# Kernel tuning notes

Hardware: AMD Instinct MI355X
Metric: run time of the kernel (lower is better)

## Reference

```python
import jax, jax.numpy as jnp
import numpy as np
import math

N_HEAD = 8


def _rope(x):
    # x: [B, H, S, D]; lucidrains rotary_embedding_torch default: interleaved pairs, theta=10000
    D = x.shape[-1]
    S = x.shape[-2]
    inv_freq = 1.0 / (10000.0 ** (jnp.arange(0, D, 2, dtype=jnp.float32) / D))  # [D/2]
    t = jnp.arange(S, dtype=jnp.float32)
    freqs = jnp.repeat(t[:, None] * inv_freq[None, :], 2, axis=-1)  # [S, D] interleaved repeat
    cos = jnp.cos(freqs).astype(x.dtype)
    sin = jnp.sin(freqs).astype(x.dtype)
    xp = x.reshape(*x.shape[:-1], D // 2, 2)
    rot = jnp.stack((-xp[..., 1], xp[..., 0]), axis=-1).reshape(x.shape)  # rotate_half (interleaved)
    return x * cos + rot * sin


def _row_linear(x, Wo):
    # faithful RowLinear: transpose then flat-reshape back (a real permutation), linear, inverse shuffle
    B, S, P = x.shape
    E = Wo.shape[0]
    x = jnp.swapaxes(x, 1, 2).reshape(B, S, P)
    x = jnp.einsum('bsp,ep->bse', x, Wo)  # [B, S, E]
    x = x.reshape(B, E, -1)  # [B, E, S]
    return jnp.swapaxes(x, 1, 2)  # [B, S, E]


def setup_inputs() -> dict:
    key = jax.random.key(0)
    k0, k1, k2, k3, k4 = jax.random.split(key, 5)
    B, S, E, P = 4, 2048, 1024, 1024
    std = 1.0 / math.sqrt(E)
    return {
        'emb': jax.random.normal(k0, (B, S, E), dtype=jnp.float32),
        'W1': jax.random.normal(k1, (P, E), dtype=jnp.float32) * std,
        'W2': jax.random.normal(k2, (P, E), dtype=jnp.float32) * std,
        'W3': jax.random.normal(k3, (P, E), dtype=jnp.float32) * std,
        'Wo': jax.random.normal(k4, (E, P), dtype=jnp.float32) * std,
    }


def reference(emb, W1, W2, W3, Wo):
    B, S, E = emb.shape
    P = W1.shape[0]
    H = N_HEAD
    D = P // H
    q = jnp.einsum('bse,pe->bsp', emb, W1).reshape(B, H, S, D)  # raw view split (as in source)
    k = jnp.einsum('bse,pe->bsp', emb, W2).reshape(B, H, S, D)
    v = jnp.einsum('bse,pe->bsp', emb, W3).reshape(B, H, S, D)
    q = _rope(q)
    k = _rope(k)
    scores = jnp.einsum('bhqd,bhkd->bhqk', q, k).astype(jnp.float32) / math.sqrt(H)
    attn = jax.nn.softmax(scores, axis=-1).astype(v.dtype)
    out = jnp.einsum('bhqk,bhkd->bhqd', attn, v)  # [B, H, S, D]
    out = jnp.swapaxes(out, 1, 2).reshape(B, S, P)
    return _row_linear(out, Wo)
```

## Files before the change

### kernel.cpp

```cpp
#include <hip/hip_runtime.h>

typedef float f32x4 __attribute__((ext_vector_type(4)));
typedef __bf16 bf16x8 __attribute__((ext_vector_type(8)));

__device__ __forceinline__ unsigned short f2bf(float f) {
  unsigned int u = __float_as_uint(f);
  u = (u + 0x7FFFu + ((u >> 16) & 1u)) >> 16;
  return (unsigned short)u;
}

__device__ __forceinline__ f32x4 mfma16(bf16x8 a, bf16x8 b, f32x4 c) {
  return __builtin_amdgcn_mfma_f32_16x16x32_bf16(a, b, c, 0, 0, 0);
}

__device__ __forceinline__ void load8_bf16(const unsigned short* p, unsigned short* d) {
  *(uint4*)d = *(const uint4*)p;
}
__device__ __forceinline__ void load8_bf16(const float* p, unsigned short* d) {
  float4 a = *(const float4*)p;
  float4 b = *(const float4*)(p + 4);
  __align__(16) unsigned short t[8] = {f2bf(a.x), f2bf(a.y), f2bf(a.z), f2bf(a.w),
                                       f2bf(b.x), f2bf(b.y), f2bf(b.z), f2bf(b.w)};
  *(uint4*)d = *(uint4*)t;
}

__device__ __forceinline__ void gload_lds16(const unsigned short* g, unsigned short* l) {
  __builtin_amdgcn_global_load_lds(
      (const __attribute__((address_space(1))) void*)g,
      (__attribute__((address_space(3))) void*)l, 16, 0, 0);
}

__global__ __launch_bounds__(256) void convert_gen(const float* __restrict__ src,
                                                   unsigned short* __restrict__ dst) {
  int idx = (blockIdx.x * 256 + threadIdx.x) * 8;
  __align__(16) unsigned short t[8];
  load8_bf16(src + idx, t);
  *(uint4*)(dst + idx) = *(uint4*)t;
}

__global__ __launch_bounds__(256) void convert_w3(const float* __restrict__ W1,
                                                  const float* __restrict__ W2,
                                                  const float* __restrict__ W3,
                                                  unsigned short* __restrict__ dst) {
  int i = blockIdx.x;
  int sel = i >> 9;
  const float* src = (sel == 0) ? W1 : (sel == 1) ? W2 : W3;
  int off = (i & 511) * 2048 + threadIdx.x * 8;
  __align__(16) unsigned short t[8];
  load8_bf16(src + off, t);
  *(uint4*)(dst + sel * 1048576 + off) = *(uint4*)t;
}

__global__ __launch_bounds__(256) void gemm_qkv(const unsigned short* __restrict__ A,
                                                const unsigned short* __restrict__ WB,
                                                unsigned short* __restrict__ q,
                                                unsigned short* __restrict__ k,
                                                unsigned short* __restrict__ v) {
  __shared__ __align__(16) unsigned short As[128][32];
  __shared__ __align__(16) unsigned short Bs[128][32];
  const int t = threadIdx.x;
  const int lane = t & 63;
  const int wid = t >> 6;
  const int quad = lane >> 4;
  const int l16 = lane & 15;
  const int wm = (wid >> 1) << 6;
  const int wn = (wid & 1) << 6;
  const int sel = blockIdx.x >> 3;
  const int nb = (blockIdx.x & 7) << 7;
  const int mbase = blockIdx.y * 128;
  const unsigned short* Bt = WB + sel * 1048576;
  unsigned short* C = (sel == 0) ? q : (sel == 1) ? k : v;

  f32x4 acc[4][4] = {};

  for (int k0 = 0; k0 < 1024; k0 += 32) {
#pragma unroll
    for (int i = 0; i < 2; ++i) {
      int c = t + (i << 8);
      int row = c >> 2;
      int col = (c & 3) << 3;
      gload_lds16(A + (size_t)(mbase + row) * 1024 + k0 + col, &As[row][col]);
      gload_lds16(Bt + (size_t)(nb + row) * 1024 + k0 + col, &Bs[row][col]);
    }
    __syncthreads();
    bf16x8 af[4], bfr[4];
#pragma unroll
    for (int mt = 0; mt < 4; ++mt)
      af[mt] = *(const bf16x8*)(&As[wm + mt * 16 + l16][quad * 8]);
#pragma unroll
    for (int nt = 0; nt < 4; ++nt)
      bfr[nt] = *(const bf16x8*)(&Bs[wn + nt * 16 + l16][quad * 8]);
#pragma unroll
    for (int mt = 0; mt < 4; ++mt)
#pragma unroll
      for (int nt = 0; nt < 4; ++nt)
        acc[mt][nt] = mfma16(af[mt], bfr[nt], acc[mt][nt]);
    __syncthreads();
  }

  const bool rope = (sel < 2);
#pragma unroll
  for (int mt = 0; mt < 4; ++mt) {
#pragma unroll
    for (int nt = 0; nt < 4; ++nt) {
#pragma unroll
      for (int r = 0; r < 4; ++r) {
        int row_g = mbase + wm + mt * 16 + quad * 4 + r;
        int col_g = nb + wn + nt * 16 + l16;
        float val = acc[mt][nt][r];
        if (rope) {
          float other = __shfl_xor(val, 1);
          int s = (((row_g & 2047) << 3) + (col_g >> 7)) & 2047;
          int d = col_g & 127;
          float invf = __expf(-0.14391156f * (float)(d >> 1));
          float ang = (float)s * invf;
          float sv, cv;
          __sincosf(ang, &sv, &cv);
          val = (d & 1) ? (val * cv + other * sv) : (val * cv - other * sv);
        }
        C[(size_t)row_g * 1024 + col_g] = f2bf(val);
      }
    }
  }
}

__global__ __launch_bounds__(256) void transpose_v(const unsigned short* __restrict__ Vn,
                                                   unsigned short* __restrict__ VT) {
  __shared__ __align__(16) unsigned short tile[64][72];
  const int t = threadIdx.x;
  const int s0 = blockIdx.x * 64;
  const int d0 = blockIdx.y * 64;
  const int bh = blockIdx.z;
  const size_t base = (size_t)bh * (2048 * 128);
#pragma unroll
  for (int i = 0; i < 2; ++i) {
    int c = t + (i << 8);
    int sr = c >> 3;
    int dc = (c & 7) << 3;
    *(uint4*)(&tile[sr][dc]) = *(const uint4*)(Vn + base + (size_t)(s0 + sr) * 128 + d0 + dc);
  }
  __syncthreads();
#pragma unroll
  for (int i = 0; i < 2; ++i) {
    int c = t + (i << 8);
    int dr = c >> 3;
    int sc = (c & 7) << 3;
    __align__(16) unsigned short tmp[8];
#pragma unroll
    for (int j = 0; j < 8; ++j) tmp[j] = tile[sc + j][dr];
    *(uint4*)(VT + base + (size_t)(d0 + dr) * 2048 + s0 + sc) = *(uint4*)tmp;
  }
}

__global__ __launch_bounds__(256) void gemm_out(const unsigned short* __restrict__ OT,
                                                const unsigned short* __restrict__ Bt,
                                                float* __restrict__ C) {
  __shared__ __align__(16) char smem_raw[128 * 68 * 4];
  auto As = (unsigned short(*)[32])smem_raw;
  auto Bs = (unsigned short(*)[32])(smem_raw + 128 * 32 * 2);
  const int t = threadIdx.x;
  const int lane = t & 63;
  const int wid = t >> 6;
  const int quad = lane >> 4;
  const int l16 = lane & 15;
  const int wm = (wid >> 1) << 6;
  const int wn = (wid & 1) << 6;
  const int mbase = blockIdx.y * 128;
  const int nbase = blockIdx.x * 128;

  f32x4 acc[4][4] = {};

  for (int k0 = 0; k0 < 1024; k0 += 32) {
#pragma unroll
    for (int i = 0; i < 2; ++i) {
      int c = t + (i << 8);
      int row = c >> 2;
      int col = (c & 3) << 3;
      int R = mbase + row;
      int b = R >> 11;
      int ii = R & 2047;
      const unsigned short* src = OT + (size_t)(b * 8 + (ii >> 8)) * (128 * 2048) +
                                  (size_t)((ii >> 1) & 127) * 2048 + ((ii & 1) << 10) +
                                  k0 + col;
      gload_lds16(src, &As[row][col]);
      gload_lds16(Bt + (size_t)(nbase + row) * 1024 + k0 + col, &Bs[row][col]);
    }
    __syncthreads();
    bf16x8 af[4], bfr[4];
#pragma unroll
    for (int mt = 0; mt < 4; ++mt)
      af[mt] = *(const bf16x8*)(&As[wm + mt * 16 + l16][quad * 8]);
#pragma unroll
    for (int nt = 0; nt < 4; ++nt)
      bfr[nt] = *(const bf16x8*)(&Bs[wn + nt * 16 + l16][quad * 8]);
#pragma unroll
    for (int mt = 0; mt < 4; ++mt)
#pragma unroll
      for (int nt = 0; nt < 4; ++nt)
        acc[mt][nt] = mfma16(af[mt], bfr[nt], acc[mt][nt]);
    __syncthreads();
  }

  float(*Ts)[68] = (float(*)[68])smem_raw;
  const int b = mbase >> 11;
  const int ebase = (mbase & 2047) >> 1;
#pragma unroll
  for (int p = 0; p < 2; ++p) {
    __syncthreads();
#pragma unroll
    for (int mt = 0; mt < 4; ++mt)
#pragma unroll
      for (int nt = 0; nt < 4; ++nt)
#pragma unroll
        for (int rr = p; rr < 4; rr += 2) {
          int col_local = wn + nt * 16 + l16;
          int row_local = wm + mt * 16 + quad * 4 + rr;
          Ts[col_local][row_local >> 1] = acc[mt][nt][rr];
        }
    __syncthreads();
    int srow = t >> 1;
    int e0 = (t & 1) << 5;
    float* dst = C + (size_t)b * 2097152 +
                 (size_t)(p * 1024 + nbase + srow) * 1024 + ebase + e0;
#pragma unroll
    for (int j = 0; j < 8; ++j)
      ((float4*)dst)[j] = *(const float4*)&Ts[srow][e0 + j * 4];
  }
}

__global__ __launch_bounds__(256, 2) void flash_attn(const unsigned short* __restrict__ Q,
                                                     const unsigned short* __restrict__ Kg,
                                                     const unsigned short* __restrict__ VTg,
                                                     unsigned short* __restrict__ OT) {
  __shared__ __align__(16) char sm[54272];
  auto Ks = (unsigned short(*)[136])sm;
  auto Vt = (unsigned short(*)[72])(sm + 17408);
  auto Ps = (unsigned short(*)[32][72])(sm + 35840);
  const int t = threadIdx.x;
  const int lane = t & 63;
  const int wid = t >> 6;
  const int quad = lane >> 4;
  const int l16 = lane & 15;
  const int i = blockIdx.x;
  const int bh = (i & 7) + ((i >> 3) & 3) * 8;
  const int qbase = (i >> 5) << 7;
  const size_t base = (size_t)bh * (2048 * 128);
  const float scale = 0.3535533905932738f;

  bf16x8 ones8;
#pragma unroll
  for (int j = 0; j < 8; ++j) ones8[j] = (__bf16)1.0f;

  bf16x8 qf[2][4];
#pragma unroll
  for (int mt = 0; mt < 2; ++mt) {
    int row = qbase + wid * 32 + mt * 16 + l16;
#pragma unroll
    for (int ks = 0; ks < 4; ++ks)
      qf[mt][ks] = *(const bf16x8*)(Q + base + (size_t)row * 128 + ks * 32 + quad * 8);
  }

  f32x4 accO[2][8] = {};
  f32x4 accL[2] = {};
  float mst[2][4];
#pragma unroll
  for (int mt = 0; mt < 2; ++mt)
#pragma unroll
    for (int r = 0; r < 4; ++r) mst[mt][r] = -__builtin_inff();

  for (int kv0 = 0; kv0 < 2048; kv0 += 64) {
#pragma unroll
    for (int i2 = 0; i2 < 4; ++i2) {
      int c = t + (i2 << 8);
      int row = c >> 4;
      int col = (c & 15) << 3;
      *(uint4*)(&Ks[row][col]) = *(const uint4*)(Kg + base + (size_t)(kv0 + row) * 128 + col);
    }
#pragma unroll
    for (int i2 = 0; i2 < 4; ++i2) {
      int c = t + (i2 << 8);
      int row = c >> 3;
      int col = (c & 7) << 3;
      *(uint4*)(&Vt[row][col]) =
          *(const uint4*)(VTg + base + (size_t)row * 2048 + kv0 + col);
    }
    __syncthreads();

    f32x4 accS[2][4];
#pragma unroll
    for (int nt = 0; nt < 4; ++nt) {
      bf16x8 kf[4];
#pragma unroll
      for (int ks = 0; ks < 4; ++ks)
        kf[ks] = *(const bf16x8*)(&Ks[nt * 16 + l16][ks * 32 + quad * 8]);
#pragma unroll
      for (int mt = 0; mt < 2; ++mt) {
        f32x4 a = {0.f, 0.f, 0.f, 0.f};
#pragma unroll
        for (int ks = 0; ks < 4; ++ks)
          a = mfma16(qf[mt][ks], kf[ks], a);
        accS[mt][nt] = a;
      }
    }

#pragma unroll
    for (int mt = 0; mt < 2; ++mt) {
#pragma unroll
      for (int r = 0; r < 4; ++r) {
        float mx = fmaxf(fmaxf(accS[mt][0][r], accS[mt][1][r]),
                         fmaxf(accS[mt][2][r], accS[mt][3][r]));
#pragma unroll
        for (int off = 1; off < 16; off <<= 1) mx = fmaxf(mx, __shfl_xor(mx, off));
        float mnew = fmaxf(mst[mt][r], mx);
        float alpha = __expf((mst[mt][r] - mnew) * scale);
        float negms = -mnew * scale;
#pragma unroll
        for (int nt = 0; nt < 4; ++nt)
          accS[mt][nt][r] = __expf(fmaf(accS[mt][nt][r], scale, negms));
        mst[mt][r] = mnew;
        accL[mt][r] *= alpha;
#pragma unroll
        for (int dt = 0; dt < 8; ++dt) accO[mt][dt][r] *= alpha;
      }
    }

#pragma unroll
    for (int mt = 0; mt < 2; ++mt)
#pragma unroll
      for (int nt = 0; nt < 4; ++nt)
#pragma unroll
        for (int r = 0; r < 4; ++r)
          Ps[wid][mt * 16 + quad * 4 + r][nt * 16 + l16] = f2bf(accS[mt][nt][r]);

    bf16x8 pf[2][2];
#pragma unroll
    for (int mt = 0; mt < 2; ++mt)
#pragma unroll
      for (int ks = 0; ks < 2; ++ks)
        pf[mt][ks] = *(const bf16x8*)(&Ps[wid][mt * 16 + l16][ks * 32 + quad * 8]);

#pragma unroll
    for (int mt = 0; mt < 2; ++mt)
#pragma unroll
      for (int ks = 0; ks < 2; ++ks)
        accL[mt] = mfma16(pf[mt][ks], ones8, accL[mt]);

#pragma unroll
    for (int dt = 0; dt < 8; ++dt) {
      bf16x8 vf[2];
#pragma unroll
      for (int ks = 0; ks < 2; ++ks)
        vf[ks] = *(const bf16x8*)(&Vt[dt * 16 + l16][ks * 32 + quad * 8]);
#pragma unroll
      for (int mt = 0; mt < 2; ++mt)
#pragma unroll
        for (int ks = 0; ks < 2; ++ks)
          accO[mt][dt] = mfma16(pf[mt][ks], vf[ks], accO[mt][dt]);
    }
    __syncthreads();
  }

  auto To = (unsigned short(*)[136])sm;
#pragma unroll
  for (int mt = 0; mt < 2; ++mt) {
#pragma unroll
    for (int r = 0; r < 4; ++r) {
      float inv = 1.f / accL[mt][r];
      int srow = wid * 32 + mt * 16 + quad * 4 + r;
#pragma unroll
      for (int dt = 0; dt < 8; ++dt)
        To[dt * 16 + l16][srow] = f2bf(accO[mt][dt][r] * inv);
    }
  }
  __syncthreads();
  int dr = t >> 1;
  int off = (t & 1) << 6;
  unsigned short* dst = OT + base + (size_t)dr * 2048 + qbase + off;
#pragma unroll
  for (int j = 0; j < 8; ++j)
    ((uint4*)dst)[j] = *(const uint4*)&To[dr][off + j * 8];
}

extern "C" void kernel_launch(void* const* d_in, const int* in_sizes, int n_in,
                              void* d_out, int out_size, void* d_ws, size_t ws_size,
                              hipStream_t stream) {
  const float* emb = (const float*)d_in[0];
  const float* W1  = (const float*)d_in[1];
  const float* W2  = (const float*)d_in[2];
  const float* W3  = (const float*)d_in[3];
  const float* Wo  = (const float*)d_in[4];
  float* out = (float*)d_out;

  const size_t NELEM = (size_t)8 * 1024 * 1024;
  unsigned short* q     = (unsigned short*)d_ws;
  unsigned short* k     = q + NELEM;
  unsigned short* vn    = k + NELEM;
  unsigned short* X     = vn + NELEM;
  unsigned short* oT    = vn;
  unsigned short* vT    = X;
  unsigned short* W123B = X;
  unsigned short* WoB   = X;
  unsigned short* embB  = (unsigned short*)d_out;

  dim3 blk(256, 1, 1);
  convert_w3<<<dim3(1536), blk, 0, stream>>>(W1, W2, W3, W123B);
  convert_gen<<<dim3(4096), blk, 0, stream>>>(emb, embB);
  gemm_qkv<<<dim3(24, 64), blk, 0, stream>>>(embB, W123B, q, k, vn);
  transpose_v<<<dim3(32, 2, 32), blk, 0, stream>>>(vn, vT);
  flash_attn<<<dim3(512, 1, 1), blk, 0, stream>>>(q, k, vT, oT);
  convert_gen<<<dim3(512), blk, 0, stream>>>(Wo, WoB);
  gemm_out<<<dim3(8, 64), blk, 0, stream>>>(oT, WoB, out);
}
```

Baseline: 362.3 us.

## Restructure flash attention with 32x32 MFMA, register P, swizzled double-buffered LDS

Rewrites the attention inner loop to use 32x32x16 bf16 MFMA computing S transposed (K as A operand), so each lane owns one query row. Softmax becomes per-lane reductions, and P is converted into the PV operand in registers via cvt_pk_bf16 and permlane32_swap instead of an LDS round trip. K/V tiles are prefetched into registers and written to a swizzled double-buffered LDS to overlap global loads with compute and avoid bank conflicts. It also adds lazy rescaling (only when the max grows by more than a threshold) and computes the row sum with scalar adds instead of a ones-MFMA. LDS rises to 64KB per block, which may affect occupancy at 2 blocks/CU.

Result: no change. 365.2 us (+0.8%).

```diff
diff --git a/kernel.cpp b/kernel.cpp
--- a/kernel.cpp
+++ b/kernel.cpp
@@ -1,6 +1,7 @@
 #include <hip/hip_runtime.h>
 
 typedef float f32x4 __attribute__((ext_vector_type(4)));
+typedef float f32x16 __attribute__((ext_vector_type(16)));
 typedef __bf16 bf16x8 __attribute__((ext_vector_type(8)));
 
 __device__ __forceinline__ unsigned short f2bf(float f) {
@@ -11,6 +12,18 @@
 
 __device__ __forceinline__ f32x4 mfma16(bf16x8 a, bf16x8 b, f32x4 c) {
   return __builtin_amdgcn_mfma_f32_16x16x32_bf16(a, b, c, 0, 0, 0);
+}
+__device__ __forceinline__ f32x16 mfma32(bf16x8 a, bf16x8 b, f32x16 c) {
+  return __builtin_amdgcn_mfma_f32_32x32x16_bf16(a, b, c, 0, 0, 0);
+}
+
+__device__ __forceinline__ unsigned int cvtpk_bf16(float a, float b) {
+  unsigned int r;
+  asm("v_cvt_pk_bf16_f32 %0, %1, %2" : "=v"(r) : "v"(a), "v"(b));
+  return r;
+}
+__device__ __forceinline__ void pl32swap(unsigned int& a, unsigned int& b) {
+  asm("v_permlane32_swap_b32 %0, %1" : "+v"(a), "+v"(b));
 }
 
 __device__ __forceinline__ void load8_bf16(const unsigned short* p, unsigned short* d) {
@@ -232,146 +245,160 @@
                                                      const unsigned short* __restrict__ Kg,
                                                      const unsigned short* __restrict__ VTg,
                                                      unsigned short* __restrict__ OT) {
-  __shared__ __align__(16) char sm[54272];
-  auto Ks = (unsigned short(*)[136])sm;
-  auto Vt = (unsigned short(*)[72])(sm + 17408);
-  auto Ps = (unsigned short(*)[32][72])(sm + 35840);
+  __shared__ __align__(16) char sm[65536];
   const int t = threadIdx.x;
   const int lane = t & 63;
   const int wid = t >> 6;
-  const int quad = lane >> 4;
-  const int l16 = lane & 15;
+  const int l31 = lane & 31;
+  const int hi = lane >> 5;
+  const int x16 = (l31 & 7) << 4;
   const int i = blockIdx.x;
   const int bh = (i & 7) + ((i >> 3) & 3) * 8;
   const int qbase = (i >> 5) << 7;
   const size_t base = (size_t)bh * (2048 * 128);
   const float scale = 0.3535533905932738f;
 
-  bf16x8 ones8;
-#pragma unroll
-  for (int j = 0; j < 8; ++j) ones8[j] = (__bf16)1.0f;
-
-  bf16x8 qf[2][4];
-#pragma unroll
-  for (int mt = 0; mt < 2; ++mt) {
-    int row = qbase + wid * 32 + mt * 16 + l16;
-#pragma unroll
-    for (int ks = 0; ks < 4; ++ks)
-      qf[mt][ks] = *(const bf16x8*)(Q + base + (size_t)row * 128 + ks * 32 + quad * 8);
-  }
-
-  f32x4 accO[2][8] = {};
-  f32x4 accL[2] = {};
-  float mst[2][4];
-#pragma unroll
-  for (int mt = 0; mt < 2; ++mt)
-#pragma unroll
-    for (int r = 0; r < 4; ++r) mst[mt][r] = -__builtin_inff();
-
-  for (int kv0 = 0; kv0 < 2048; kv0 += 64) {
-#pragma unroll
-    for (int i2 = 0; i2 < 4; ++i2) {
-      int c = t + (i2 << 8);
-      int row = c >> 4;
-      int col = (c & 15) << 3;
-      *(uint4*)(&Ks[row][col]) = *(const uint4*)(Kg + base + (size_t)(kv0 + row) * 128 + col);
-    }
-#pragma unroll
-    for (int i2 = 0; i2 < 4; ++i2) {
-      int c = t + (i2 << 8);
-      int row = c >> 3;
-      int col = (c & 7) << 3;
-      *(uint4*)(&Vt[row][col]) =
-          *(const uint4*)(VTg + base + (size_t)row * 2048 + kv0 + col);
-    }
-    __syncthreads();
-
-    f32x4 accS[2][4];
-#pragma unroll
-    for (int nt = 0; nt < 4; ++nt) {
-      bf16x8 kf[4];
-#pragma unroll
-      for (int ks = 0; ks < 4; ++ks)
-        kf[ks] = *(const bf16x8*)(&Ks[nt * 16 + l16][ks * 32 + quad * 8]);
-#pragma unroll
-      for (int mt = 0; mt < 2; ++mt) {
-        f32x4 a = {0.f, 0.f, 0.f, 0.f};
-#pragma unroll
-        for (int ks = 0; ks < 4; ++ks)
-          a = mfma16(qf[mt][ks], kf[ks], a);
-        accS[mt][nt] = a;
+  bf16x8 qf[8];
+  {
+    const unsigned short* qp = Q + base + (size_t)(qbase + wid * 32 + l31) * 128 + hi * 8;
+#pragma unroll
+    for (int ks = 0; ks < 8; ++ks) qf[ks] = *(const bf16x8*)(qp + ks * 16);
+  }
+
+  f32x16 accO[4] = {};
+  float m = -__builtin_inff();
+  float l = 0.f;
+
+  uint4 kreg[4], vreg[4];
+  const unsigned short* Kg_b = Kg + base;
+  const unsigned short* Vg_b = VTg + base;
+
+#pragma unroll
+  for (int j = 0; j < 4; ++j) {
+    int c = t + (j << 8);
+    kreg[j] = *(const uint4*)(Kg_b + (size_t)(c >> 4) * 128 + ((c & 15) << 3));
+    vreg[j] = *(const uint4*)(Vg_b + (size_t)(c >> 3) * 2048 + ((c & 7) << 3));
+  }
+  {
+    unsigned short* Kw = (unsigned short*)sm;
+    unsigned short* Vw = (unsigned short*)(sm + 16384);
+#pragma unroll
+    for (int j = 0; j < 4; ++j) {
+      int c = t + (j << 8);
+      int r = c >> 4, ch = c & 15;
+      *(uint4*)(Kw + r * 128 + ((ch ^ (r & 7)) << 3)) = kreg[j];
+      int d = c >> 3, cv = c & 7;
+      *(uint4*)(Vw + d * 64 + ((cv ^ (d & 7)) << 3)) = vreg[j];
+    }
+  }
+  __syncthreads();
+
+  int cur = 0;
+  for (int kv = 0; kv < 2048; kv += 64) {
+    const bool nxt = (kv + 64) < 2048;
+    if (nxt) {
+#pragma unroll
+      for (int j = 0; j < 4; ++j) {
+        int c = t + (j << 8);
+        kreg[j] = *(const uint4*)(Kg_b + (size_t)(kv + 64 + (c >> 4)) * 128 + ((c & 15) << 3));
+        vreg[j] = *(const uint4*)(Vg_b + (size_t)(c >> 3) * 2048 + (kv + 64) + ((c & 7) << 3));
       }
     }
-
-#pragma unroll
-    for (int mt = 0; mt < 2; ++mt) {
-#pragma unroll
-      for (int r = 0; r < 4; ++r) {
-        float mx = fmaxf(fmaxf(accS[mt][0][r], accS[mt][1][r]),
-                         fmaxf(accS[mt][2][r], accS[mt][3][r]));
-#pragma unroll
-        for (int off = 1; off < 16; off <<= 1) mx = fmaxf(mx, __shfl_xor(mx, off));
-        float mnew = fmaxf(mst[mt][r], mx);
-        float alpha = __expf((mst[mt][r] - mnew) * scale);
-        float negms = -mnew * scale;
-#pragma unroll
-        for (int nt = 0; nt < 4; ++nt)
-          accS[mt][nt][r] = __expf(fmaf(accS[mt][nt][r], scale, negms));
-        mst[mt][r] = mnew;
-        accL[mt][r] *= alpha;
-#pragma unroll
-        for (int dt = 0; dt < 8; ++dt) accO[mt][dt][r] *= alpha;
+    const char* Kb = sm + (cur << 15);
+    const char* Vb = Kb + 16384;
+
+    f32x16 s0 = {}, s1 = {};
+#pragma unroll
+    for (int ks = 0; ks < 8; ++ks) {
+      int cb = (ks * 32 + hi * 16) ^ x16;
+      bf16x8 k0 = *(const bf16x8*)(Kb + l31 * 256 + cb);
+      bf16x8 k1 = *(const bf16x8*)(Kb + 8192 + l31 * 256 + cb);
+      s0 = mfma32(k0, qf[ks], s0);
+      s1 = mfma32(k1, qf[ks], s1);
+    }
+
+    float mx = s0[0];
+#pragma unroll
+    for (int r = 1; r < 16; ++r) mx = fmaxf(mx, s0[r]);
+#pragma unroll
+    for (int r = 0; r < 16; ++r) mx = fmaxf(mx, s1[r]);
+    mx = fmaxf(mx, __shfl_xor(mx, 32));
+    if (__any(mx > m + 16.f)) {
+      float mnew = fmaxf(m, mx);
+      float alpha = __expf((m - mnew) * scale);
+      l *= alpha;
+#pragma unroll
+      for (int dt = 0; dt < 4; ++dt)
+#pragma unroll
+        for (int r = 0; r < 16; ++r) accO[dt][r] *= alpha;
+      m = mnew;
+    }
+    float negms = -m * scale;
+    float ps = 0.f;
+#pragma unroll
+    for (int r = 0; r < 16; ++r) {
+      s0[r] = __expf(fmaf(s0[r], scale, negms));
+      ps += s0[r];
+    }
+#pragma unroll
+    for (int r = 0; r < 16; ++r) {
+      s1[r] = __expf(fmaf(s1[r], scale, negms));
+      ps += s1[r];
+    }
+    ps += __shfl_xor(ps, 32);
+    l += ps;
+
+    bf16x8 pfrag[4];
+#pragma unroll
+    for (int kb = 0; kb < 4; ++kb) {
+      const f32x16& S = (kb < 2) ? s0 : s1;
+      const int b = (kb & 1) * 8;
+      unsigned int a0 = cvtpk_bf16(S[b + 0], S[b + 1]);
+      unsigned int a1 = cvtpk_bf16(S[b + 2], S[b + 3]);
+      unsigned int a2 = cvtpk_bf16(S[b + 4], S[b + 5]);
+      unsigned int a3 = cvtpk_bf16(S[b + 6], S[b + 7]);
+      pl32swap(a0, a2);
+      pl32swap(a1, a3);
+      union { unsigned int u[4]; bf16x8 v; } pu;
+      pu.u[0] = a0; pu.u[1] = a1; pu.u[2] = a2; pu.u[3] = a3;
+      pfrag[kb] = pu.v;
+    }
+
+#pragma unroll
+    for (int dt = 0; dt < 4; ++dt) {
+#pragma unroll
+      for (int kb = 0; kb < 4; ++kb) {
+        bf16x8 vfr = *(const bf16x8*)(Vb + l31 * 128 + dt * 4096 + ((kb * 32 + hi * 16) ^ x16));
+        accO[dt] = mfma32(vfr, pfrag[kb], accO[dt]);
       }
     }
 
-#pragma unroll
-    for (int mt = 0; mt < 2; ++mt)
-#pragma unroll
-      for (int nt = 0; nt < 4; ++nt)
-#pragma unroll
-        for (int r = 0; r < 4; ++r)
-          Ps[wid][mt * 16 + quad * 4 + r][nt * 16 + l16] = f2bf(accS[mt][nt][r]);
-
-    bf16x8 pf[2][2];
-#pragma unroll
-    for (int mt = 0; mt < 2; ++mt)
-#pragma unroll
-      for (int ks = 0; ks < 2; ++ks)
-        pf[mt][ks] = *(const bf16x8*)(&Ps[wid][mt * 16 + l16][ks * 32 + quad * 8]);
-
-#pragma unroll
-    for (int mt = 0; mt < 2; ++mt)
-#pragma unroll
-      for (int ks = 0; ks < 2; ++ks)
-        accL[mt] = mfma16(pf[mt][ks], ones8, accL[mt]);
-
-#pragma unroll
-    for (int dt = 0; dt < 8; ++dt) {
-      bf16x8 vf[2];
-#pragma unroll
-      for (int ks = 0; ks < 2; ++ks)
-        vf[ks] = *(const bf16x8*)(&Vt[dt * 16 + l16][ks * 32 + quad * 8]);
-#pragma unroll
-      for (int mt = 0; mt < 2; ++mt)
-#pragma unroll
-        for (int ks = 0; ks < 2; ++ks)
-          accO[mt][dt] = mfma16(pf[mt][ks], vf[ks], accO[mt][dt]);
-    }
-    __syncthreads();
+    if (nxt) {
+      unsigned short* Kw = (unsigned short*)(sm + ((cur ^ 1) << 15));
+      unsigned short* Vw = (unsigned short*)((char*)Kw + 16384);
+#pragma unroll
+      for (int j = 0; j < 4; ++j) {
+        int c = t + (j << 8);
+        int r = c >> 4, ch = c & 15;
+        *(uint4*)(Kw + r * 128 + ((ch ^ (r & 7)) << 3)) = kreg[j];
+        int d = c >> 3, cv = c & 7;
+        *(uint4*)(Vw + d * 64 + ((cv ^ (d & 7)) << 3)) = vreg[j];
+      }
+    }
+    __syncthreads();
+    cur ^= 1;
   }
 
   auto To = (unsigned short(*)[136])sm;
-#pragma unroll
-  for (int mt = 0; mt < 2; ++mt) {
-#pragma unroll
-    for (int r = 0; r < 4; ++r) {
-      float inv = 1.f / accL[mt][r];
-      int srow = wid * 32 + mt * 16 + quad * 4 + r;
-#pragma unroll
-      for (int dt = 0; dt < 8; ++dt)
-        To[dt * 16 + l16][srow] = f2bf(accO[mt][dt][r] * inv);
-    }
-  }
+  const float invl = 1.f / l;
+  const int qloc = wid * 32 + l31;
+#pragma unroll
+  for (int dt = 0; dt < 4; ++dt)
+#pragma unroll
+    for (int r = 0; r < 16; ++r) {
+      int d = dt * 32 + (r & 3) + ((r >> 2) << 3) + hi * 4;
+      To[d][qloc] = f2bf(accO[dt][r] * invl);
+    }
   __syncthreads();
   int dr = t >> 1;
   int off = (t & 1) << 6;
```
